# Performance work log

Measured on AMD Instinct MI355X. Metric: run time of the kernel, lower is better.

Reference implementation:

```python
import jax, jax.numpy as jnp
import numpy as np

B, T, E, H = 2, 4096, 768, 12
D = E // H  # head_dim = 64


def setup_inputs() -> dict:
    key = jax.random.key(0)
    ks = jax.random.split(key, 9)
    s = 1.0 / np.sqrt(E)
    return {
        "x": jax.random.normal(ks[0], (B, T, E), dtype=jnp.float32),
        "wq": jax.random.normal(ks[1], (E, E), dtype=jnp.float32) * s,
        "bq": jnp.zeros((E,), dtype=jnp.float32),
        "wk": jax.random.normal(ks[2], (E, E), dtype=jnp.float32) * s,
        "bk": jnp.zeros((E,), dtype=jnp.float32),
        "wv": jax.random.normal(ks[3], (E, E), dtype=jnp.float32) * s,
        "bv": jnp.zeros((E,), dtype=jnp.float32),
        "wo": jax.random.normal(ks[4], (E, E), dtype=jnp.float32) * s,
        "bo": jnp.zeros((E,), dtype=jnp.float32),
    }


def reference(x, wq, bq, wk, bk, wv, bv, wo, bo):
    # Linear projections (torch Linear: x @ W.T + b; weights here stored as (in,out))
    q = x @ wq + bq  # (B,T,E)
    k = x @ wk + bk
    v = x @ wv + bv

    def split(t):
        return t.reshape(B, T, H, D).transpose(0, 2, 1, 3)  # (B,H,T,D)

    q, k, v = split(q), split(k), split(v)
    scale = 1.0 / np.sqrt(D).astype(np.float32)
    scores = jnp.einsum("bhtd,bhsd->bhts", q, k) * scale  # (B,H,T,T)
    causal = jnp.tril(jnp.ones((T, T), dtype=bool))
    scores = jnp.where(causal, scores, -jnp.inf)
    attn = jax.nn.softmax(scores, axis=-1)
    out = jnp.einsum("bhts,bhsd->bhtd", attn, v)  # (B,H,T,D)
    out = out.transpose(0, 2, 1, 3).reshape(B, T, E)
    return out @ wo + bo
```

## Files before the change

### kernel.cpp

```cpp
#include <hip/hip_runtime.h>
#include <hip/hip_bf16.h>

#define TSEQ 4096
#define EMB 768
#define NH 12
#define DH 64
#define BT 8192

typedef __attribute__((ext_vector_type(8))) short bf16x8;
typedef __attribute__((ext_vector_type(4))) float f32x4;

#define FENCE() asm volatile("" ::: "memory")

__device__ __forceinline__ f32x4 mfma16(bf16x8 a, bf16x8 b, f32x4 c) {
    return __builtin_amdgcn_mfma_f32_16x16x32_bf16(a, b, c, 0, 0, 0);
}

__device__ __forceinline__ void gload16(const void* g, void* l) {
    __builtin_amdgcn_global_load_lds((const __attribute__((address_space(1))) void*)g,
                                     (__attribute__((address_space(3))) void*)l, 16, 0, 0);
}

__global__ __launch_bounds__(256) void conv_all_k(const float* __restrict__ x,
                                                  __hip_bfloat16* __restrict__ xb,
                                                  const float* w0, const float* w1,
                                                  const float* w2, const float* w3,
                                                  __hip_bfloat16* o0, __hip_bfloat16* o1,
                                                  __hip_bfloat16* o2, __hip_bfloat16* o3) {
    __shared__ float tile[32][33];
    int bid = blockIdx.x;
    if (bid < 6144) {
        int i = (bid * 256 + threadIdx.x) * 4;
        float4 v = *(const float4*)(x + i);
        union { unsigned short u[4]; uint2 p; } o;
        __hip_bfloat16 t0 = __float2bfloat16(v.x); o.u[0] = *(unsigned short*)&t0;
        __hip_bfloat16 t1 = __float2bfloat16(v.y); o.u[1] = *(unsigned short*)&t1;
        __hip_bfloat16 t2 = __float2bfloat16(v.z); o.u[2] = *(unsigned short*)&t2;
        __hip_bfloat16 t3 = __float2bfloat16(v.w); o.u[3] = *(unsigned short*)&t3;
        *(uint2*)(xb + i) = o.p;
        return;
    }
    bid -= 6144;
    const int z = bid / 576, rr = bid % 576, by = rr / 24, bx = rr % 24;
    const float* w; __hip_bfloat16* o;
    switch (z) {
        case 0: w = w0; o = o0; break;
        case 1: w = w1; o = o1; break;
        case 2: w = w2; o = o2; break;
        default: w = w3; o = o3; break;
    }
    int tx = threadIdx.x & 31, ty = threadIdx.x >> 5;
    int kb = by * 32, nb = bx * 32;
    for (int i = 0; i < 32; i += 8)
        tile[ty + i][tx] = w[(size_t)(kb + ty + i) * EMB + nb + tx];
    __syncthreads();
    for (int i = 0; i < 32; i += 8)
        o[(size_t)(nb + ty + i) * EMB + kb + tx] = __float2bfloat16(tile[tx][ty + i]);
}

__device__ __forceinline__ void gemm_body(const __hip_bfloat16* __restrict__ A,
                                          const __hip_bfloat16* __restrict__ Wt,
                                          const float* __restrict__ bias,
                                          void* __restrict__ outp, int mode, float scale) {
    __shared__ alignas(16) char As[2][8192];
    __shared__ alignas(16) char Bs[2][8192];
    const int m0 = blockIdx.x * 128, n0 = blockIdx.y * 128;
    const int tid = threadIdx.x;
    const int lane = tid & 63, l15 = lane & 15, lg = lane >> 4;
    const int wave = tid >> 6, wm = wave >> 1, wn = wave & 1;
    const int swz = (l15 & 7) << 4;

    int mrow_[2]; int kelem_[2];
#pragma unroll
    for (int c = 0; c < 2; ++c) {
        int p = c * 4096 + tid * 16;
        int lrow = p >> 7, w = p & 127;
        int wp = w ^ ((lrow & 7) << 4);
        mrow_[c] = lrow + ((wp >> 6) & 1) * 64;
        kelem_[c] = (wp & 63) >> 1;
    }

    f32x4 acc[4][4];
    for (int i = 0; i < 4; ++i)
        for (int j = 0; j < 4; ++j) acc[i][j] = (f32x4){0.f, 0.f, 0.f, 0.f};

    auto stage = [&](int buf, int k0) {
#pragma unroll
        for (int c = 0; c < 2; ++c)
            gload16(A + (size_t)(m0 + mrow_[c]) * EMB + k0 + kelem_[c],
                    As[buf] + c * 4096 + wave * 1024);
#pragma unroll
        for (int c = 0; c < 2; ++c)
            gload16(Wt + (size_t)(n0 + mrow_[c]) * EMB + k0 + kelem_[c],
                    Bs[buf] + c * 4096 + wave * 1024);
    };

    stage(0, 0);
    const int NK = EMB / 32;
    for (int ks = 0; ks < NK; ++ks) {
        const int cur = ks & 1;
        asm volatile("s_waitcnt vmcnt(0)" ::: "memory");
        FENCE(); __builtin_amdgcn_s_barrier(); FENCE();
        if (ks + 1 < NK) stage(cur ^ 1, (ks + 1) * 32);
        bf16x8 af[4], bfv[4];
#pragma unroll
        for (int f = 0; f < 4; ++f)
            af[f] = *(const bf16x8*)(As[cur] + (f * 16 + l15) * 128 + ((wm * 64 + lg * 16) ^ swz));
#pragma unroll
        for (int f = 0; f < 4; ++f)
            bfv[f] = *(const bf16x8*)(Bs[cur] + (f * 16 + l15) * 128 + ((wn * 64 + lg * 16) ^ swz));
        __builtin_amdgcn_s_setprio(1);
#pragma unroll
        for (int i = 0; i < 4; ++i)
#pragma unroll
            for (int j = 0; j < 4; ++j)
                acc[i][j] = mfma16(af[i], bfv[j], acc[i][j]);
        __builtin_amdgcn_s_setprio(0);
    }

#pragma unroll
    for (int i = 0; i < 4; ++i) {
#pragma unroll
        for (int j = 0; j < 4; ++j) {
            const int n = n0 + wn * 64 + j * 16 + l15;
            const float bv = bias[n];
            const int mbase = m0 + wm * 64 + i * 16 + lg * 4;
#pragma unroll
            for (int r = 0; r < 4; ++r) {
                const int m = mbase + r;
                const float val = (acc[i][j][r] + bv) * scale;
                if (mode == 2) {
                    ((float*)outp)[(size_t)m * EMB + n] = val;
                } else {
                    const int b = m >> 12, t = m & (TSEQ - 1);
                    const int h = n >> 6, d = n & 63;
                    size_t addr;
                    if (mode == 0) addr = ((size_t)(b * NH + h) * TSEQ + t) * DH + d;
                    else           addr = ((size_t)(b * NH + h) * DH + d) * TSEQ + t;
                    ((__hip_bfloat16*)outp)[addr] = __float2bfloat16(val);
                }
            }
        }
    }
}

__global__ __launch_bounds__(256) void qkv_k(const __hip_bfloat16* __restrict__ xb,
                                             const __hip_bfloat16* __restrict__ wqT,
                                             const __hip_bfloat16* __restrict__ wkT,
                                             const __hip_bfloat16* __restrict__ wvT,
                                             const float* __restrict__ bq,
                                             const float* __restrict__ bk,
                                             const float* __restrict__ bv,
                                             __hip_bfloat16* __restrict__ qo,
                                             __hip_bfloat16* __restrict__ ko,
                                             __hip_bfloat16* __restrict__ vo) {
    const __hip_bfloat16* Wt; const float* bias; void* o; int mode; float scale;
    const float cq = 0.125f * 1.44269504089f;
    switch (blockIdx.z) {
        case 0:  Wt = wqT; bias = bq; o = qo; mode = 0; scale = cq;  break;
        case 1:  Wt = wkT; bias = bk; o = ko; mode = 0; scale = 1.f; break;
        default: Wt = wvT; bias = bv; o = vo; mode = 1; scale = 1.f; break;
    }
    gemm_body(xb, Wt, bias, o, mode, scale);
}

__global__ __launch_bounds__(256) void oproj64_k(const __hip_bfloat16* __restrict__ A,
                                                 const __hip_bfloat16* __restrict__ Wt,
                                                 const float* __restrict__ bias,
                                                 float* __restrict__ out) {
    __shared__ alignas(16) char As[2][4096];
    __shared__ alignas(16) char Bs[2][8192];
    const int m0 = blockIdx.x * 64, n0 = blockIdx.y * 128;
    const int tid = threadIdx.x;
    const int lane = tid & 63, l15 = lane & 15, lg = lane >> 4;
    const int wave = tid >> 6, wm = wave >> 1, wn = wave & 1;
    const int swz = (l15 & 7) << 4;

    int amrow, akelem;
    {
        int p = tid * 16;
        int lrow = p >> 7, w = p & 127;
        int wp = w ^ ((lrow & 7) << 4);
        amrow = lrow + ((wp >> 6) & 1) * 32;
        akelem = (wp & 63) >> 1;
    }
    int bnrow[2], bkelem[2];
#pragma unroll
    for (int c = 0; c < 2; ++c) {
        int p = c * 4096 + tid * 16;
        int lrow = p >> 7, w = p & 127;
        int wp = w ^ ((lrow & 7) << 4);
        bnrow[c] = lrow + ((wp >> 6) & 1) * 64;
        bkelem[c] = (wp & 63) >> 1;
    }

    f32x4 acc[2][4];
    for (int i = 0; i < 2; ++i)
        for (int j = 0; j < 4; ++j) acc[i][j] = (f32x4){0.f, 0.f, 0.f, 0.f};

    auto stage = [&](int buf, int k0) {
        gload16(A + (size_t)(m0 + amrow) * EMB + k0 + akelem,
                As[buf] + wave * 1024);
#pragma unroll
        for (int c = 0; c < 2; ++c)
            gload16(Wt + (size_t)(n0 + bnrow[c]) * EMB + k0 + bkelem[c],
                    Bs[buf] + c * 4096 + wave * 1024);
    };

    stage(0, 0);
    const int NK = EMB / 32;
    for (int ks = 0; ks < NK; ++ks) {
        const int cur = ks & 1;
        asm volatile("s_waitcnt vmcnt(0)" ::: "memory");
        FENCE(); __builtin_amdgcn_s_barrier(); FENCE();
        if (ks + 1 < NK) stage(cur ^ 1, (ks + 1) * 32);
        bf16x8 af[2], bfv[4];
#pragma unroll
        for (int f = 0; f < 2; ++f)
            af[f] = *(const bf16x8*)(As[cur] + (f * 16 + l15) * 128 + ((wm * 64 + lg * 16) ^ swz));
#pragma unroll
        for (int f = 0; f < 4; ++f)
            bfv[f] = *(const bf16x8*)(Bs[cur] + (f * 16 + l15) * 128 + ((wn * 64 + lg * 16) ^ swz));
        __builtin_amdgcn_s_setprio(1);
#pragma unroll
        for (int i = 0; i < 2; ++i)
#pragma unroll
            for (int j = 0; j < 4; ++j)
                acc[i][j] = mfma16(af[i], bfv[j], acc[i][j]);
        __builtin_amdgcn_s_setprio(0);
    }

#pragma unroll
    for (int i = 0; i < 2; ++i) {
#pragma unroll
        for (int j = 0; j < 4; ++j) {
            const int n = n0 + wn * 64 + j * 16 + l15;
            const float bv = bias[n];
            const int mbase = m0 + wm * 32 + i * 16 + lg * 4;
#pragma unroll
            for (int r = 0; r < 4; ++r)
                out[(size_t)(mbase + r) * EMB + n] = acc[i][j][r] + bv;
        }
    }
}

__global__ __launch_bounds__(256, 3) void attn_k(const __hip_bfloat16* __restrict__ qb,
                                                 const __hip_bfloat16* __restrict__ kb,
                                                 const __hip_bfloat16* __restrict__ vt,
                                                 __hip_bfloat16* __restrict__ ab) {
    __shared__ alignas(16) char Ks[2][8192];
    __shared__ alignas(16) char Vs[2][8192];
    __shared__ alignas(16) char pbuf[4][4096];
    const int lane = threadIdx.x & 63, l15 = lane & 15, lg = lane >> 4;
    const int wave = threadIdx.x >> 6;
    const int bid = blockIdx.x;
    const int xcd = bid & 7, slot = bid >> 3;
    const int pair = slot & 31, hgrp = slot >> 5;
    const int bh = xcd + hgrp * 8;
    const __hip_bfloat16* Qh = qb + (size_t)bh * TSEQ * DH;
    const __hip_bfloat16* Kh = kb + (size_t)bh * TSEQ * DH;
    const __hip_bfloat16* Vh = vt + (size_t)bh * DH * TSEQ;
    char* Pb = pbuf[wave];
    const int swz = (l15 & 7) << 4;
    const int b = bh / NH, h = bh % NH;
    const float M0 = 12.0f;

    bf16x8 ones8;
#pragma unroll
    for (int j = 0; j < 8; ++j) ones8[j] = (short)0x3F80;

    unsigned ka[8];
#pragma unroll
    for (int st = 0; st < 4; ++st)
#pragma unroll
        for (int ks = 0; ks < 2; ++ks)
            ka[st * 2 + ks] = (unsigned)((st * 16 + l15) * 128 + ((ks * 64 + lg * 16) ^ swz));
    char* pwh[4]; char* prh[2]; char* pwl[4]; char* prl[2];
#pragma unroll
    for (int st = 0; st < 4; ++st) {
        pwh[st] = Pb + l15 * 128 + ((st * 32 + lg * 8) ^ swz);
        pwl[st] = pwh[st] + 2048;
    }
#pragma unroll
    for (int ks = 0; ks < 2; ++ks) {
        prh[ks] = Pb + l15 * 128 + ((ks * 64 + lg * 16) ^ swz);
        prl[ks] = prh[ks] + 2048;
    }
    const int dthr = wave * 16 + l15 - lg * 4;

    int r_[2], wp_[2];
#pragma unroll
    for (int c = 0; c < 2; ++c) {
        int p = c * 4096 + wave * 1024 + lane * 16;
        int r = p >> 7, w = p & 127;
        r_[c] = r;
        wp_[c] = (w ^ ((r & 7) << 4)) >> 1;
    }

    const int lo = pair, hi = 63 - pair;
    const int q0l = lo * 64 + wave * 16;
    const int q0h = hi * 64 + wave * 16;
    const int nsb = hi + 1;

    bf16x8 qh0 = *(const bf16x8*)(Qh + (size_t)(q0h + l15) * DH + lg * 8);
    bf16x8 qh1 = *(const bf16x8*)(Qh + (size_t)(q0h + l15) * DH + 32 + lg * 8);
    bf16x8 ql0 = *(const bf16x8*)(Qh + (size_t)(q0l + l15) * DH + lg * 8);
    bf16x8 ql1 = *(const bf16x8*)(Qh + (size_t)(q0l + l15) * DH + 32 + lg * 8);

    f32x4 oh[4], ol[4];
#pragma unroll
    for (int dt = 0; dt < 4; ++dt) { oh[dt] = (f32x4){0.f,0.f,0.f,0.f}; ol[dt] = (f32x4){0.f,0.f,0.f,0.f}; }
    f32x4 lh = (f32x4){0.f,0.f,0.f,0.f}, ll = (f32x4){0.f,0.f,0.f,0.f};

    const char* kg0 = (const char*)(Kh + (size_t)r_[0] * DH + wp_[0]);
    const char* kg1 = (const char*)(Kh + (size_t)r_[1] * DH + wp_[1]);
    const char* vg0 = (const char*)(Vh + (size_t)r_[0] * TSEQ + wp_[0]);
    const char* vg1 = (const char*)(Vh + (size_t)r_[1] * TSEQ + wp_[1]);

#define STAGE(DST) do {                                                          \
    gload16(kg0, Ks[DST] + wave * 1024);                                         \
    gload16(kg1, Ks[DST] + 4096 + wave * 1024);                                  \
    gload16(vg0, Vs[DST] + wave * 1024);                                         \
    gload16(vg1, Vs[DST] + 4096 + wave * 1024);                                  \
    kg0 += 8192; kg1 += 8192; vg0 += 128; vg1 += 128;                            \
} while (0)

#define QKSM(KF, Q0, Q1, MASKB, PW) do {                                         \
    f32x4 sa[4];                                                                 \
    __builtin_amdgcn_s_setprio(1);                                               \
    _Pragma("unroll")                                                            \
    for (int st = 0; st < 4; ++st) {                                             \
        f32x4 z = (f32x4){0.f, 0.f, 0.f, 0.f};                                   \
        z = mfma16(KF[st * 2 + 0], Q0, z);                                       \
        z = mfma16(KF[st * 2 + 1], Q1, z);                                       \
        sa[st] = z;                                                              \
    }                                                                            \
    __builtin_amdgcn_s_setprio(0);                                               \
    if (MASKB) {                                                                 \
        _Pragma("unroll")                                                        \
        for (int st = 0; st < 4; ++st)                                           \
            _Pragma("unroll")                                                    \
            for (int r = 0; r < 4; ++r)                                          \
                if (st * 16 + r > dthr) sa[st][r] = -INFINITY;                   \
    }                                                                            \
    _Pragma("unroll")                                                            \
    for (int st = 0; st < 4; ++st) {                                             \
        const float e0 = exp2f(sa[st][0] - M0);                                  \
        const float e1 = exp2f(sa[st][1] - M0);                                  \
        const float e2 = exp2f(sa[st][2] - M0);                                  \
        const float e3 = exp2f(sa[st][3] - M0);                                  \
        uint2 pkv;                                                               \
        asm("v_cvt_pk_bf16_f32 %0, %1, %2" : "=v"(pkv.x) : "v"(e0), "v"(e1));    \
        asm("v_cvt_pk_bf16_f32 %0, %1, %2" : "=v"(pkv.y) : "v"(e2), "v"(e3));    \
        *(uint2*)PW[st] = pkv;                                                   \
    }                                                                            \
} while (0)

#define PVU(VF, OV, LA, PR) do {                                                 \
    bf16x8 pf0 = *(const bf16x8*)PR[0];                                          \
    bf16x8 pf1 = *(const bf16x8*)PR[1];                                          \
    __builtin_amdgcn_s_setprio(1);                                               \
    LA = mfma16(pf0, ones8, LA);                                                 \
    LA = mfma16(pf1, ones8, LA);                                                 \
    _Pragma("unroll")                                                            \
    for (int dt = 0; dt < 4; ++dt)                                               \
        OV[dt] = mfma16(pf0, VF[dt * 2 + 0], OV[dt]);                            \
    _Pragma("unroll")                                                            \
    for (int dt = 0; dt < 4; ++dt)                                               \
        OV[dt] = mfma16(pf1, VF[dt * 2 + 1], OV[dt]);                            \
    __builtin_amdgcn_s_setprio(0);                                               \
} while (0)

#define SBODY(BUF, PRE, LOACT, MHI, MLO) do {                                    \
    asm volatile("s_waitcnt vmcnt(0)" ::: "memory");                             \
    FENCE(); __builtin_amdgcn_s_barrier(); FENCE();                              \
    if (PRE) STAGE((BUF) ^ 1);                                                   \
    bf16x8 kf[8];                                                                \
    _Pragma("unroll")                                                            \
    for (int i = 0; i < 8; ++i) kf[i] = *(const bf16x8*)(Ks[BUF] + ka[i]);       \
    QKSM(kf, qh0, qh1, MHI, pwh);                                                \
    if (LOACT) QKSM(kf, ql0, ql1, MLO, pwl);                                     \
    bf16x8 vf[8];                                                                \
    _Pragma("unroll")                                                            \
    for (int i = 0; i < 8; ++i) vf[i] = *(const bf16x8*)(Vs[BUF] + ka[i]);       \
    asm volatile("s_waitcnt lgkmcnt(0)" ::: "memory");                           \
    PVU(vf, oh, lh, prh);                                                        \
    if (LOACT) PVU(vf, ol, ll, prl);                                             \
} while (0)

    STAGE(0);
    int sb = 0;
    while (sb + 2 <= nsb) {
        SBODY(0, true, sb <= lo, false, sb == lo);
        SBODY(1, sb + 2 < nsb, sb + 1 <= lo, sb + 1 == nsb - 1, sb + 1 == lo);
        sb += 2;
    }
    if (sb < nsb) SBODY(0, false, sb <= lo, true, sb == lo);

#undef SBODY
#undef PVU
#undef QKSM
#undef STAGE

    {
        float inv[4];
#pragma unroll
        for (int r = 0; r < 4; ++r) inv[r] = 1.0f / lh[r];
#pragma unroll
        for (int r = 0; r < 4; ++r) {
            const int qrow = q0h + lg * 4 + r;
            const size_t rowbase = ((size_t)b * TSEQ + qrow) * EMB + h * DH;
#pragma unroll
            for (int dt = 0; dt < 4; ++dt)
                ab[rowbase + dt * 16 + l15] = __float2bfloat16(oh[dt][r] * inv[r]);
        }
    }
    {
        float inv[4];
#pragma unroll
        for (int r = 0; r < 4; ++r) inv[r] = 1.0f / ll[r];
#pragma unroll
        for (int r = 0; r < 4; ++r) {
            const int qrow = q0l + lg * 4 + r;
            const size_t rowbase = ((size_t)b * TSEQ + qrow) * EMB + h * DH;
#pragma unroll
            for (int dt = 0; dt < 4; ++dt)
                ab[rowbase + dt * 16 + l15] = __float2bfloat16(ol[dt][r] * inv[r]);
        }
    }
}

extern "C" void kernel_launch(void* const* d_in, const int* in_sizes, int n_in,
                              void* d_out, int out_size, void* d_ws, size_t ws_size,
                              hipStream_t stream) {
    (void)in_sizes; (void)n_in; (void)out_size; (void)ws_size;
    const float* x  = (const float*)d_in[0];
    const float* wq = (const float*)d_in[1];
    const float* bq = (const float*)d_in[2];
    const float* wk = (const float*)d_in[3];
    const float* bk = (const float*)d_in[4];
    const float* wv = (const float*)d_in[5];
    const float* bv = (const float*)d_in[6];
    const float* wo = (const float*)d_in[7];
    const float* bo = (const float*)d_in[8];
    float* out = (float*)d_out;

    char* ws = (char*)d_ws;
    size_t off = 0;
    auto alloc = [&](size_t bytes) {
        char* p = ws + off;
        off += (bytes + 255) & ~(size_t)255;
        return p;
    };
    __hip_bfloat16* xb  = (__hip_bfloat16*)alloc((size_t)BT * EMB * 2);
    __hip_bfloat16* qbf = (__hip_bfloat16*)alloc((size_t)BT * EMB * 2);
    __hip_bfloat16* kbf = (__hip_bfloat16*)alloc((size_t)BT * EMB * 2);
    __hip_bfloat16* vtb = (__hip_bfloat16*)alloc((size_t)BT * EMB * 2);
    __hip_bfloat16* abf = (__hip_bfloat16*)alloc((size_t)BT * EMB * 2);
    __hip_bfloat16* wqT = (__hip_bfloat16*)alloc((size_t)EMB * EMB * 2);
    __hip_bfloat16* wkT = (__hip_bfloat16*)alloc((size_t)EMB * EMB * 2);
    __hip_bfloat16* wvT = (__hip_bfloat16*)alloc((size_t)EMB * EMB * 2);
    __hip_bfloat16* woT = (__hip_bfloat16*)alloc((size_t)EMB * EMB * 2);

    conv_all_k<<<6144 + 2304, 256, 0, stream>>>(x, xb, wq, wk, wv, wo, wqT, wkT, wvT, woT);
    qkv_k<<<dim3(64, 6, 3), 256, 0, stream>>>(xb, wqT, wkT, wvT, bq, bk, bv, qbf, kbf, vtb);
    attn_k<<<768, 256, 0, stream>>>(qbf, kbf, vtb, abf);
    oproj64_k<<<dim3(128, 6), 256, 0, stream>>>(abf, woT, bo, out);
}
```

Measured before the change: 186.0 us.

## Split attention KV range by parity across two blocks and combine partials

New measurement: 324.4 us. +74.4%, slower.

```diff
diff --git a/kernel.cpp b/kernel.cpp
--- a/kernel.cpp
+++ b/kernel.cpp
@@ -6,6 +6,7 @@
 #define NH 12
 #define DH 64
 #define BT 8192
+#define NROWS (24 * TSEQ)
 
 typedef __attribute__((ext_vector_type(8))) short bf16x8;
 typedef __attribute__((ext_vector_type(4))) float f32x4;
@@ -244,25 +245,27 @@
     }
 }
 
-__global__ __launch_bounds__(256, 3) void attn_k(const __hip_bfloat16* __restrict__ qb,
+__global__ __launch_bounds__(256, 5) void attn_k(const __hip_bfloat16* __restrict__ qb,
                                                  const __hip_bfloat16* __restrict__ kb,
                                                  const __hip_bfloat16* __restrict__ vt,
-                                                 __hip_bfloat16* __restrict__ ab) {
-    __shared__ alignas(16) char Ks[2][8192];
-    __shared__ alignas(16) char Vs[2][8192];
+                                                 __hip_bfloat16* __restrict__ opart,
+                                                 float* __restrict__ lpart) {
+    __shared__ alignas(16) char Ks[8192];
+    __shared__ alignas(16) char Vs[8192];
     __shared__ alignas(16) char pbuf[4][4096];
     const int lane = threadIdx.x & 63, l15 = lane & 15, lg = lane >> 4;
     const int wave = threadIdx.x >> 6;
     const int bid = blockIdx.x;
     const int xcd = bid & 7, slot = bid >> 3;
-    const int pair = slot & 31, hgrp = slot >> 5;
+    const int pair = slot & 31;
+    const int parity = (slot >> 5) & 1;
+    const int hgrp = slot >> 6;
     const int bh = xcd + hgrp * 8;
     const __hip_bfloat16* Qh = qb + (size_t)bh * TSEQ * DH;
     const __hip_bfloat16* Kh = kb + (size_t)bh * TSEQ * DH;
     const __hip_bfloat16* Vh = vt + (size_t)bh * DH * TSEQ;
     char* Pb = pbuf[wave];
     const int swz = (l15 & 7) << 4;
-    const int b = bh / NH, h = bh % NH;
     const float M0 = 12.0f;
 
     bf16x8 ones8;
@@ -312,17 +315,17 @@
     for (int dt = 0; dt < 4; ++dt) { oh[dt] = (f32x4){0.f,0.f,0.f,0.f}; ol[dt] = (f32x4){0.f,0.f,0.f,0.f}; }
     f32x4 lh = (f32x4){0.f,0.f,0.f,0.f}, ll = (f32x4){0.f,0.f,0.f,0.f};
 
-    const char* kg0 = (const char*)(Kh + (size_t)r_[0] * DH + wp_[0]);
-    const char* kg1 = (const char*)(Kh + (size_t)r_[1] * DH + wp_[1]);
-    const char* vg0 = (const char*)(Vh + (size_t)r_[0] * TSEQ + wp_[0]);
-    const char* vg1 = (const char*)(Vh + (size_t)r_[1] * TSEQ + wp_[1]);
-
-#define STAGE(DST) do {                                                          \
-    gload16(kg0, Ks[DST] + wave * 1024);                                         \
-    gload16(kg1, Ks[DST] + 4096 + wave * 1024);                                  \
-    gload16(vg0, Vs[DST] + wave * 1024);                                         \
-    gload16(vg1, Vs[DST] + 4096 + wave * 1024);                                  \
-    kg0 += 8192; kg1 += 8192; vg0 += 128; vg1 += 128;                            \
+    const char* kg0 = (const char*)(Kh + (size_t)r_[0] * DH + wp_[0]) + parity * 8192;
+    const char* kg1 = (const char*)(Kh + (size_t)r_[1] * DH + wp_[1]) + parity * 8192;
+    const char* vg0 = (const char*)(Vh + (size_t)r_[0] * TSEQ + wp_[0]) + parity * 128;
+    const char* vg1 = (const char*)(Vh + (size_t)r_[1] * TSEQ + wp_[1]) + parity * 128;
+
+#define STAGE() do {                                                             \
+    gload16(kg0, Ks + wave * 1024);                                              \
+    gload16(kg1, Ks + 4096 + wave * 1024);                                       \
+    gload16(vg0, Vs + wave * 1024);                                              \
+    gload16(vg1, Vs + 4096 + wave * 1024);                                       \
+    kg0 += 16384; kg1 += 16384; vg0 += 256; vg1 += 256;                          \
 } while (0)
 
 #define QKSM(KF, Q0, Q1, MASKB, PW) do {                                         \
@@ -371,63 +374,79 @@
     __builtin_amdgcn_s_setprio(0);                                               \
 } while (0)
 
-#define SBODY(BUF, PRE, LOACT, MHI, MLO) do {                                    \
-    asm volatile("s_waitcnt vmcnt(0)" ::: "memory");                             \
-    FENCE(); __builtin_amdgcn_s_barrier(); FENCE();                              \
-    if (PRE) STAGE((BUF) ^ 1);                                                   \
-    bf16x8 kf[8];                                                                \
-    _Pragma("unroll")                                                            \
-    for (int i = 0; i < 8; ++i) kf[i] = *(const bf16x8*)(Ks[BUF] + ka[i]);       \
-    QKSM(kf, qh0, qh1, MHI, pwh);                                                \
-    if (LOACT) QKSM(kf, ql0, ql1, MLO, pwl);                                     \
-    bf16x8 vf[8];                                                                \
-    _Pragma("unroll")                                                            \
-    for (int i = 0; i < 8; ++i) vf[i] = *(const bf16x8*)(Vs[BUF] + ka[i]);       \
-    asm volatile("s_waitcnt lgkmcnt(0)" ::: "memory");                           \
-    PVU(vf, oh, lh, prh);                                                        \
-    if (LOACT) PVU(vf, ol, ll, prl);                                             \
-} while (0)
-
-    STAGE(0);
-    int sb = 0;
-    while (sb + 2 <= nsb) {
-        SBODY(0, true, sb <= lo, false, sb == lo);
-        SBODY(1, sb + 2 < nsb, sb + 1 <= lo, sb + 1 == nsb - 1, sb + 1 == lo);
-        sb += 2;
-    }
-    if (sb < nsb) SBODY(0, false, sb <= lo, true, sb == lo);
-
-#undef SBODY
+    STAGE();
+    for (int sb = parity; sb < nsb; sb += 2) {
+        const bool loact = (sb <= lo);
+        asm volatile("s_waitcnt vmcnt(0)" ::: "memory");
+        FENCE(); __builtin_amdgcn_s_barrier(); FENCE();
+        bf16x8 kf[8];
+#pragma unroll
+        for (int i = 0; i < 8; ++i) kf[i] = *(const bf16x8*)(Ks + ka[i]);
+        QKSM(kf, qh0, qh1, (sb == hi), pwh);
+        if (loact) QKSM(kf, ql0, ql1, (sb == lo), pwl);
+        bf16x8 vf[8];
+#pragma unroll
+        for (int i = 0; i < 8; ++i) vf[i] = *(const bf16x8*)(Vs + ka[i]);
+        asm volatile("s_waitcnt lgkmcnt(0)" ::: "memory");
+        FENCE(); __builtin_amdgcn_s_barrier(); FENCE();
+        if (sb + 2 < nsb) STAGE();
+        PVU(vf, oh, lh, prh);
+        if (loact) PVU(vf, ol, ll, prl);
+    }
+
 #undef PVU
 #undef QKSM
 #undef STAGE
 
+    const size_t prow = ((size_t)parity * 24 + bh) * TSEQ;
     {
-        float inv[4];
-#pragma unroll
-        for (int r = 0; r < 4; ++r) inv[r] = 1.0f / lh[r];
 #pragma unroll
         for (int r = 0; r < 4; ++r) {
-            const int qrow = q0h + lg * 4 + r;
-            const size_t rowbase = ((size_t)b * TSEQ + qrow) * EMB + h * DH;
+            const size_t base = (prow + q0h + lg * 4 + r) * DH;
 #pragma unroll
             for (int dt = 0; dt < 4; ++dt)
-                ab[rowbase + dt * 16 + l15] = __float2bfloat16(oh[dt][r] * inv[r]);
+                opart[base + dt * 16 + l15] = __float2bfloat16(oh[dt][r]);
+        }
+        if (l15 == 0) {
+#pragma unroll
+            for (int r = 0; r < 4; ++r) lpart[prow + q0h + lg * 4 + r] = lh[r];
         }
     }
     {
-        float inv[4];
-#pragma unroll
-        for (int r = 0; r < 4; ++r) inv[r] = 1.0f / ll[r];
 #pragma unroll
         for (int r = 0; r < 4; ++r) {
-            const int qrow = q0l + lg * 4 + r;
-            const size_t rowbase = ((size_t)b * TSEQ + qrow) * EMB + h * DH;
+            const size_t base = (prow + q0l + lg * 4 + r) * DH;
 #pragma unroll
             for (int dt = 0; dt < 4; ++dt)
-                ab[rowbase + dt * 16 + l15] = __float2bfloat16(ol[dt][r] * inv[r]);
-        }
-    }
+                opart[base + dt * 16 + l15] = __float2bfloat16(ol[dt][r]);
+        }
+        if (l15 == 0) {
+#pragma unroll
+            for (int r = 0; r < 4; ++r) lpart[prow + q0l + lg * 4 + r] = ll[r];
+        }
+    }
+}
+
+__global__ __launch_bounds__(256) void comb_k(const __hip_bfloat16* __restrict__ opart,
+                                              const float* __restrict__ lpart,
+                                              __hip_bfloat16* __restrict__ ab) {
+    const int idx = blockIdx.x * 256 + threadIdx.x;
+    const int row = idx >> 3;
+    const int d0 = (idx & 7) * 8;
+    const int bh = row >> 12, qrow = row & 4095;
+    const int b_ = bh / NH, h = bh % NH;
+    bf16x8 a0 = *(const bf16x8*)(opart + (size_t)row * DH + d0);
+    bf16x8 a1 = *(const bf16x8*)(opart + ((size_t)NROWS + row) * DH + d0);
+    const float linv = 1.0f / (lpart[row] + lpart[NROWS + row]);
+    union { unsigned short u[8]; uint4 v; } o;
+#pragma unroll
+    for (int j = 0; j < 8; ++j) {
+        const float v0 = __uint_as_float(((unsigned)(unsigned short)a0[j]) << 16);
+        const float v1 = __uint_as_float(((unsigned)(unsigned short)a1[j]) << 16);
+        __hip_bfloat16 hb = __float2bfloat16((v0 + v1) * linv);
+        o.u[j] = *(unsigned short*)&hb;
+    }
+    *(uint4*)(ab + ((size_t)(b_ * TSEQ + qrow)) * EMB + h * DH + d0) = o.v;
 }
 
 extern "C" void kernel_launch(void* const* d_in, const int* in_sizes, int n_in,
@@ -452,18 +471,21 @@
         off += (bytes + 255) & ~(size_t)255;
         return p;
     };
-    __hip_bfloat16* xb  = (__hip_bfloat16*)alloc((size_t)BT * EMB * 2);
-    __hip_bfloat16* qbf = (__hip_bfloat16*)alloc((size_t)BT * EMB * 2);
-    __hip_bfloat16* kbf = (__hip_bfloat16*)alloc((size_t)BT * EMB * 2);
-    __hip_bfloat16* vtb = (__hip_bfloat16*)alloc((size_t)BT * EMB * 2);
-    __hip_bfloat16* abf = (__hip_bfloat16*)alloc((size_t)BT * EMB * 2);
-    __hip_bfloat16* wqT = (__hip_bfloat16*)alloc((size_t)EMB * EMB * 2);
-    __hip_bfloat16* wkT = (__hip_bfloat16*)alloc((size_t)EMB * EMB * 2);
-    __hip_bfloat16* wvT = (__hip_bfloat16*)alloc((size_t)EMB * EMB * 2);
-    __hip_bfloat16* woT = (__hip_bfloat16*)alloc((size_t)EMB * EMB * 2);
+    __hip_bfloat16* xb   = (__hip_bfloat16*)alloc((size_t)BT * EMB * 2);
+    __hip_bfloat16* qbf  = (__hip_bfloat16*)alloc((size_t)BT * EMB * 2);
+    __hip_bfloat16* kbf  = (__hip_bfloat16*)alloc((size_t)BT * EMB * 2);
+    __hip_bfloat16* vtb  = (__hip_bfloat16*)alloc((size_t)BT * EMB * 2);
+    __hip_bfloat16* abf  = (__hip_bfloat16*)alloc((size_t)BT * EMB * 2);
+    __hip_bfloat16* wqT  = (__hip_bfloat16*)alloc((size_t)EMB * EMB * 2);
+    __hip_bfloat16* wkT  = (__hip_bfloat16*)alloc((size_t)EMB * EMB * 2);
+    __hip_bfloat16* wvT  = (__hip_bfloat16*)alloc((size_t)EMB * EMB * 2);
+    __hip_bfloat16* woT  = (__hip_bfloat16*)alloc((size_t)EMB * EMB * 2);
+    __hip_bfloat16* opart = (__hip_bfloat16*)alloc((size_t)2 * NROWS * DH * 2);
+    float*          lpart = (float*)alloc((size_t)2 * NROWS * 4);
 
     conv_all_k<<<6144 + 2304, 256, 0, stream>>>(x, xb, wq, wk, wv, wo, wqT, wkT, wvT, woT);
     qkv_k<<<dim3(64, 6, 3), 256, 0, stream>>>(xb, wqT, wkT, wvT, bq, bk, bv, qbf, kbf, vtb);
-    attn_k<<<768, 256, 0, stream>>>(qbf, kbf, vtb, abf);
+    attn_k<<<1536, 256, 0, stream>>>(qbf, kbf, vtb, opart, lpart);
+    comb_k<<<NROWS * 8 / 256, 256, 0, stream>>>(opart, lpart, abf);
     oproj64_k<<<dim3(128, 6), 256, 0, stream>>>(abf, woT, bo, out);
 }
```
